# Optimization experiments

Hardware: AMD Instinct MI355X
Metric: run time of the kernel (lower is better)

The kernel has to match this reference:

```python
import jax, jax.numpy as jnp
import numpy as np

H, D, C, K, N, B = 16, 64, 1024, 256, 4096, 2

def setup_inputs() -> dict:
    key = jax.random.key(0)
    ks = jax.random.split(key, 10)
    s = lambda k, shp, fan: jax.random.normal(k, shp, jnp.float32) * (1.0 / np.sqrt(fan))
    return {
        "x": jax.random.normal(ks[0], (B, N, C), jnp.float32),
        "Wq": s(ks[1], (H, D, C), C),   # per-head Linear(channels->dim), no bias
        "Wk": s(ks[2], (H, D, C), C),
        "Wv": s(ks[3], (H, D, C), C),
        "We": s(ks[4], (H, K, N), N),   # E: Linear(input_size->dim_k)
        "bE": jnp.zeros((H, K), jnp.float32),
        "Wf": s(ks[5], (H, K, N), N),   # F: Linear(input_size->dim_k)
        "bF": jnp.zeros((H, K), jnp.float32),
        "Wo": s(ks[6], (C, H * D), H * D),
        "bo": jnp.zeros((C,), jnp.float32),
    }

def reference(x, Wq, Wk, Wv, We, bE, Wf, bF, Wo, bo):
    b, n, c = x.shape
    h, d = Wq.shape[0], Wq.shape[1]
    # per-head Q/K/V projections, vectorized over heads: [b,h,n,d]
    Q = jnp.einsum('bnc,hdc->bhnd', x, Wq)
    Kt = jnp.einsum('bnc,hdc->bhdn', x, Wk)   # K already transposed(1,2)
    Vt = jnp.einsum('bnc,hdc->bhdn', x, Wv)   # V transposed(1,2)
    # Linformer E/F low-rank projections along sequence axis -> [b,h,d,k]
    Ke = jnp.einsum('bhdn,hkn->bhdk', Kt, We) + bE[None, :, None, :]
    Vf = jnp.einsum('bhdn,hkn->bhdk', Vt, Wf) + bF[None, :, None, :]
    # scaled scores + softmax over low-rank dim k
    scores = jnp.einsum('bhnd,bhdk->bhnk', Q, Kt if False else Ke) / jnp.sqrt(jnp.asarray(d, x.dtype))
    P = jax.nn.softmax(scores, axis=-1)
    # P @ V_f^T  -> [b,h,n,d]
    out = jnp.einsum('bhnk,bhkd->bhnd', P, jnp.swapaxes(Vf, -1, -2))
    # concat heads -> [b,n,h*d]
    out = jnp.transpose(out, (0, 2, 1, 3)).reshape(b, n, h * d)
    out = jax.nn.gelu(out, approximate=False)
    return out @ Wo.T + bo
```

## Files before the change

kernel.cpp:

```cpp
#include <hip/hip_runtime.h>

typedef unsigned short u16;
typedef float f32x4 __attribute__((ext_vector_type(4)));
typedef short s16x8 __attribute__((ext_vector_type(8)));
typedef unsigned short u16x4 __attribute__((ext_vector_type(4)));

__device__ __forceinline__ u16 f2bf(float f) {
  union { float f; unsigned u; } v; v.f = f;
  unsigned r = v.u + 0x7FFFu + ((v.u >> 16) & 1u);
  return (u16)(r >> 16);
}

__device__ __forceinline__ void gload_lds16(const void* g, void* l) {
  __builtin_amdgcn_global_load_lds(
      (const __attribute__((address_space(1))) void*)g,
      (__attribute__((address_space(3))) void*)l, 16, 0, 0);
}

__global__ __launch_bounds__(256) void cast_f32_bf16(
    const float* __restrict__ src, u16* __restrict__ dst, int n4) {
  int i = blockIdx.x * 256 + threadIdx.x;
  if (i >= n4) return;
  f32x4 v = ((const f32x4*)src)[i];
  u16x4 o = { f2bf(v[0]), f2bf(v[1]), f2bf(v[2]), f2bf(v[3]) };
  ((u16x4*)dst)[i] = o;
}

template <int FINAL>
__global__ __launch_bounds__(256) void gemm_bt(
    const u16* __restrict__ A, const u16* __restrict__ B,
    void* __restrict__ Cout, const float* __restrict__ bias,
    int K, int lda, int ldb, int ldc) {
  __shared__ u16 As[128 * 32];
  __shared__ u16 Bs[128 * 32];
  const int tid = threadIdx.x;
  const int wid = tid >> 6, lane = tid & 63;
  const int lo = lane & 15, hi = lane >> 4;
  const int wr = wid >> 1, wc = wid & 1;
  const long brow = (long)blockIdx.y * 128;
  const long bcol = (long)blockIdx.x * 128;

  f32x4 acc[4][4] = {};

  const char* Ab = (const char*)(A + (size_t)brow * lda);
  const char* Bb = (const char*)(B + (size_t)bcol * ldb);
  const int ldab = lda * 2, ldbb = ldb * 2;

  for (int k0 = 0; k0 < K; k0 += 32) {
#pragma unroll
    for (int i = 0; i < 2; ++i) {
      int ob = wid * 2048 + i * 1024;
      int o = ob + lane * 16;
      int row = o >> 6, cb = o & 63;
      gload_lds16(Ab + (size_t)row * ldab + k0 * 2 + cb, (char*)As + ob);
      gload_lds16(Bb + (size_t)row * ldbb + k0 * 2 + cb, (char*)Bs + ob);
    }
    __syncthreads();
    s16x8 af[4], bfr[4];
#pragma unroll
    for (int m = 0; m < 4; ++m)
      af[m] = *(const s16x8*)&As[(wr * 64 + m * 16 + lo) * 32 + hi * 8];
#pragma unroll
    for (int n = 0; n < 4; ++n)
      bfr[n] = *(const s16x8*)&Bs[(wc * 64 + n * 16 + lo) * 32 + hi * 8];
#pragma unroll
    for (int m = 0; m < 4; ++m)
#pragma unroll
      for (int n = 0; n < 4; ++n)
        acc[m][n] = __builtin_amdgcn_mfma_f32_16x16x32_bf16(af[m], bfr[n], acc[m][n], 0, 0, 0);
    __syncthreads();
  }
#pragma unroll
  for (int m = 0; m < 4; ++m) {
#pragma unroll
    for (int n = 0; n < 4; ++n) {
#pragma unroll
      for (int r = 0; r < 4; ++r) {
        size_t row = brow + wr * 64 + m * 16 + hi * 4 + r;
        size_t col = bcol + wc * 64 + n * 16 + lo;
        float v = acc[m][n][r];
        if (FINAL) ((float*)Cout)[row * ldc + col] = v + bias[col];
        else       ((u16*)Cout)[row * ldc + col] = f2bf(v);
      }
    }
  }
}

__global__ __launch_bounds__(256) void kevf_kernel(
    const float* __restrict__ We, const float* __restrict__ Wf,
    const u16* __restrict__ QKV, float* __restrict__ part) {
  __shared__ u16 Wa[64 * 32];
  __shared__ u16 Vt[64 * 32];
  const int type = blockIdx.z >> 2, ns = blockIdx.z & 3;
  const int bh = blockIdx.y, b = bh >> 4, h = bh & 15;
  const int kk0 = blockIdx.x * 64;
  const float* W = (type ? Wf : We) + ((size_t)(h * 256 + kk0)) * 4096;
  const int col0 = (type ? 2048 : 1024) + h * 64;
  const int tid = threadIdx.x, wid = tid >> 6, lane = tid & 63;
  const int lo = lane & 15, hi = lane >> 4;

  f32x4 acc[4] = {};

  const int nbeg = ns << 10, nend = nbeg + 1024;
  for (int n0 = nbeg; n0 < nend; n0 += 32) {
    {
      int r = tid >> 2, c8 = (tid & 3) * 8;
      const f32x4* wp = (const f32x4*)(W + (size_t)r * 4096 + n0 + c8);
      f32x4 v0 = wp[0], v1 = wp[1];
      s16x8 wv;
      wv[0] = (short)f2bf(v0[0]); wv[1] = (short)f2bf(v0[1]);
      wv[2] = (short)f2bf(v0[2]); wv[3] = (short)f2bf(v0[3]);
      wv[4] = (short)f2bf(v1[0]); wv[5] = (short)f2bf(v1[1]);
      wv[6] = (short)f2bf(v1[2]); wv[7] = (short)f2bf(v1[3]);
      *(s16x8*)((char*)Wa + r * 64 + ((c8 * 2) ^ ((r & 3) << 4))) = wv;
    }
    {
      int n = tid >> 3, dd0 = (tid & 7) * 8;
      s16x8 v = *(const s16x8*)(QKV + (size_t)(b * 4096 + n0 + n) * 3072 + col0 + dd0);
#pragma unroll
      for (int q = 0; q < 8; ++q) {
        int dd = dd0 + q;
        Vt[dd * 32 + (n ^ (((dd >> 3) & 3) << 3))] = (u16)v[q];
      }
    }
    __syncthreads();
    int rr = wid * 16 + lo;
    s16x8 a = *(const s16x8*)((const char*)Wa + rr * 64 + ((hi * 16) ^ ((rr & 3) << 4)));
#pragma unroll
    for (int dt = 0; dt < 4; ++dt) {
      int dd = dt * 16 + lo;
      s16x8 bv = *(const s16x8*)&Vt[dd * 32 + ((hi * 8) ^ (((dd >> 3) & 3) << 3))];
      acc[dt] = __builtin_amdgcn_mfma_f32_16x16x32_bf16(a, bv, acc[dt], 0, 0, 0);
    }
    __syncthreads();
  }
  const size_t pbase = ((size_t)((type * 32 + bh) * 4 + blockIdx.x) * 4 + ns) * 4096;
#pragma unroll
  for (int dt = 0; dt < 4; ++dt)
#pragma unroll
    for (int r = 0; r < 4; ++r) {
      int kkl = wid * 16 + hi * 4 + r;
      int dd = dt * 16 + lo;
      part[pbase + kkl * 64 + dd] = acc[dt][r];
    }
}

__global__ __launch_bounds__(256) void kevf_reduce(
    const float* __restrict__ part, const float* __restrict__ bE,
    const float* __restrict__ bF, u16* __restrict__ KeT, u16* __restrict__ Vf) {
  const int tb = blockIdx.x;
  const int type = tb >> 7, bh = (tb >> 2) & 31, kc = tb & 3;
  const int t = threadIdx.x;
  const int kkl = t >> 2, dd0 = (t & 3) * 16;
  const float* p = part + (size_t)tb * 16384 + kkl * 64 + dd0;
  f32x4 s[4];
#pragma unroll
  for (int j = 0; j < 4; ++j) s[j] = ((const f32x4*)p)[j];
#pragma unroll
  for (int ns = 1; ns < 4; ++ns)
#pragma unroll
    for (int j = 0; j < 4; ++j) {
      f32x4 v = ((const f32x4*)(p + ns * 4096))[j];
      s[j][0] += v[0]; s[j][1] += v[1]; s[j][2] += v[2]; s[j][3] += v[3];
    }
  const int kk = kc * 64 + kkl;
  const float bias = (type ? bF : bE)[(bh & 15) * 256 + kk];
  if (type == 0) {
    u16* o = KeT + ((size_t)bh * 256 + kk) * 64 + dd0;
#pragma unroll
    for (int j = 0; j < 4; ++j) {
      u16x4 w = { f2bf(s[j][0] + bias), f2bf(s[j][1] + bias),
                  f2bf(s[j][2] + bias), f2bf(s[j][3] + bias) };
      *(u16x4*)(o + j * 4) = w;
    }
  } else {
#pragma unroll
    for (int j = 0; j < 4; ++j)
#pragma unroll
      for (int e = 0; e < 4; ++e) {
        int dd = dd0 + j * 4 + e;
        Vf[((size_t)bh * 64 + dd) * 256 + kk] = f2bf(s[j][e] + bias);
      }
  }
}

__global__ __launch_bounds__(256) void attn_fused(
    const u16* __restrict__ QKV, const u16* __restrict__ KeT,
    const u16* __restrict__ Vf, u16* __restrict__ attn) {
  __shared__ char smem[65536];
  char* sKe = smem;
  char* sVf = smem + 32768;
  const int tid = threadIdx.x, wid = tid >> 6, lane = tid & 63;
  const int lo = lane & 15, hi = lane >> 4;
  const int bh = blockIdx.y, b = bh >> 4, h = bh & 15;
  const int n0 = blockIdx.x * 64;

  const char* keg = (const char*)(KeT + (size_t)bh * 256 * 64);
  const char* vfg = (const char*)(Vf + (size_t)bh * 64 * 256);
#pragma unroll
  for (int i = 0; i < 8; ++i) {
    int ob = wid * 8192 + i * 1024;
    int o = ob + lane * 16;
    int kr = o >> 7, kc = o & 127;
    gload_lds16(keg + kr * 128 + (kc ^ ((kr & 7) << 4)), sKe + ob);
    int vr = o >> 9, vc = o & 511;
    gload_lds16(vfg + vr * 512 + (vc ^ ((vr & 7) << 4)), sVf + ob);
  }
  const u16* qp = QKV + (size_t)(b * 4096 + n0 + wid * 16 + lo) * 3072 + h * 64;
  s16x8 qf0 = *(const s16x8*)(qp + hi * 8);
  s16x8 qf1 = *(const s16x8*)(qp + 32 + hi * 8);
  __syncthreads();

  f32x4 sc[16];
#pragma unroll
  for (int nt = 0; nt < 16; ++nt) {
    int kk = nt * 16 + lo;
    int sw = (kk & 7) << 4;
    s16x8 b0 = *(const s16x8*)(sKe + kk * 128 + ((hi * 16) ^ sw));
    s16x8 b1 = *(const s16x8*)(sKe + kk * 128 + ((64 + hi * 16) ^ sw));
    f32x4 c = {0.f, 0.f, 0.f, 0.f};
    c = __builtin_amdgcn_mfma_f32_16x16x32_bf16(qf0, b0, c, 0, 0, 0);
    c = __builtin_amdgcn_mfma_f32_16x16x32_bf16(qf1, b1, c, 0, 0, 0);
    sc[nt] = c;
  }
  float mx[4], inv[4];
#pragma unroll
  for (int r = 0; r < 4; ++r) {
    float m = sc[0][r];
#pragma unroll
    for (int nt = 1; nt < 16; ++nt) m = fmaxf(m, sc[nt][r]);
    m = fmaxf(m, __shfl_xor(m, 1));
    m = fmaxf(m, __shfl_xor(m, 2));
    m = fmaxf(m, __shfl_xor(m, 4));
    m = fmaxf(m, __shfl_xor(m, 8));
    mx[r] = m;
  }
  const float SCL = 0.125f * 1.4426950408889634f;
  float sm[4] = {0.f, 0.f, 0.f, 0.f};
#pragma unroll
  for (int nt = 0; nt < 16; ++nt)
#pragma unroll
    for (int r = 0; r < 4; ++r) {
      float p = exp2f((sc[nt][r] - mx[r]) * SCL);
      sc[nt][r] = p;
      sm[r] += p;
    }
#pragma unroll
  for (int r = 0; r < 4; ++r) {
    float s = sm[r];
    s += __shfl_xor(s, 1);
    s += __shfl_xor(s, 2);
    s += __shfl_xor(s, 4);
    s += __shfl_xor(s, 8);
    inv[r] = 1.0f / s;
  }
  __syncthreads();
  char* pb = smem + wid * 8192;
#pragma unroll
  for (int nt = 0; nt < 16; ++nt)
#pragma unroll
    for (int r = 0; r < 4; ++r) {
      int row = hi * 4 + r;
      int kk = nt * 16 + lo;
      *(u16*)(pb + row * 512 + ((kk * 2) ^ ((row & 7) << 4))) = f2bf(sc[nt][r] * inv[r]);
    }
  __syncthreads();
  s16x8 pa[8];
#pragma unroll
  for (int ks = 0; ks < 8; ++ks)
    pa[ks] = *(const s16x8*)(pb + lo * 512 + ((ks * 64 + hi * 16) ^ ((lo & 7) << 4)));
#pragma unroll
  for (int dt = 0; dt < 4; ++dt) {
    int dd = dt * 16 + lo;
    int sw = (dd & 7) << 4;
    f32x4 o = {0.f, 0.f, 0.f, 0.f};
#pragma unroll
    for (int ks = 0; ks < 8; ++ks) {
      s16x8 vb = *(const s16x8*)(sVf + dd * 512 + ((ks * 64 + hi * 16) ^ sw));
      o = __builtin_amdgcn_mfma_f32_16x16x32_bf16(pa[ks], vb, o, 0, 0, 0);
    }
#pragma unroll
    for (int r = 0; r < 4; ++r) {
      int row = n0 + wid * 16 + hi * 4 + r;
      float x = o[r];
      float g = 0.5f * x * (1.0f + erff(x * 0.7071067811865476f));
      attn[(size_t)(b * 4096 + row) * 1024 + h * 64 + dd] = f2bf(g);
    }
  }
}

extern "C" void kernel_launch(void* const* d_in, const int* in_sizes, int n_in,
                              void* d_out, int out_size, void* d_ws, size_t ws_size,
                              hipStream_t stream) {
  const float* x  = (const float*)d_in[0];
  const float* Wq = (const float*)d_in[1];
  const float* Wk = (const float*)d_in[2];
  const float* Wv = (const float*)d_in[3];
  const float* We = (const float*)d_in[4];
  const float* bE = (const float*)d_in[5];
  const float* Wf = (const float*)d_in[6];
  const float* bF = (const float*)d_in[7];
  const float* Wo = (const float*)d_in[8];
  const float* bo = (const float*)d_in[9];
  float* out = (float*)d_out;

  char* ws = (char*)d_ws;
  u16* xb   = (u16*)(ws);
  u16* Wqkv = (u16*)(ws + 16777216);
  u16* Wob  = (u16*)(ws + 23068672);
  u16* QKV  = (u16*)(ws + 25165824);
  u16* KeT  = (u16*)(ws + 75497472);
  u16* Vf   = (u16*)(ws + 76546048);
  u16* attn = (u16*)(ws + 77594624);
  float* part = (float*)(ws);

  cast_f32_bf16<<<8192, 256, 0, stream>>>(x, xb, 2097152);
  cast_f32_bf16<<<1024, 256, 0, stream>>>(Wq, Wqkv, 262144);
  cast_f32_bf16<<<1024, 256, 0, stream>>>(Wk, Wqkv + 1048576, 262144);
  cast_f32_bf16<<<1024, 256, 0, stream>>>(Wv, Wqkv + 2097152, 262144);
  cast_f32_bf16<<<1024, 256, 0, stream>>>(Wo, Wob, 262144);

  gemm_bt<0><<<dim3(24, 64), 256, 0, stream>>>(xb, Wqkv, QKV, nullptr,
                                               1024, 1024, 1024, 3072);
  kevf_kernel<<<dim3(4, 32, 8), 256, 0, stream>>>(We, Wf, QKV, part);
  kevf_reduce<<<256, 256, 0, stream>>>(part, bE, bF, KeT, Vf);
  attn_fused<<<dim3(64, 32), 256, 0, stream>>>(QKV, KeT, Vf, attn);
  gemm_bt<1><<<dim3(8, 64), 256, 0, stream>>>(attn, Wob, out, bo,
                                              1024, 1024, 1024, 1024);
}
```

Measured before the change: 223.7 us.

## Replace GEMM with 4-stage pipelined, swizzled LDS kernel using 128x256 tiles

Replaces the synchronous single-buffer bf16 GEMM with a 4-stage ring of LDS buffers. Three k-tiles are prefetched ahead via global_load_lds, with vmcnt waits and a single barrier per iteration. The block tile grows to 128x256 with 8 waves, and an XOR swizzle on LDS column offsets is meant to reduce bank conflicts on fragment reads. The goal is to hide global-load latency behind MFMA work in the QKV and output projections, at the cost of more LDS per block and fewer blocks in flight.

```diff
diff --git a/kernel.cpp b/kernel.cpp
--- a/kernel.cpp
+++ b/kernel.cpp
@@ -27,57 +27,92 @@
 }
 
 template <int FINAL>
-__global__ __launch_bounds__(256) void gemm_bt(
+__global__ __launch_bounds__(512) void gemm_pipe(
     const u16* __restrict__ A, const u16* __restrict__ B,
     void* __restrict__ Cout, const float* __restrict__ bias,
     int K, int lda, int ldb, int ldc) {
-  __shared__ u16 As[128 * 32];
-  __shared__ u16 Bs[128 * 32];
+  __shared__ char smem[4 * 8192 + 4 * 16384];
+  char* sA = smem;
+  char* sB = smem + 32768;
   const int tid = threadIdx.x;
   const int wid = tid >> 6, lane = tid & 63;
   const int lo = lane & 15, hi = lane >> 4;
-  const int wr = wid >> 1, wc = wid & 1;
+  const int wm = wid >> 2, wn = wid & 3;
   const long brow = (long)blockIdx.y * 128;
-  const long bcol = (long)blockIdx.x * 128;
+  const long bcol = (long)blockIdx.x * 256;
+  const int T = K >> 5;
 
   f32x4 acc[4][4] = {};
 
   const char* Ab = (const char*)(A + (size_t)brow * lda);
   const char* Bb = (const char*)(B + (size_t)bcol * ldb);
-  const int ldab = lda * 2, ldbb = ldb * 2;
-
-  for (int k0 = 0; k0 < K; k0 += 32) {
-#pragma unroll
-    for (int i = 0; i < 2; ++i) {
-      int ob = wid * 2048 + i * 1024;
-      int o = ob + lane * 16;
-      int row = o >> 6, cb = o & 63;
-      gload_lds16(Ab + (size_t)row * ldab + k0 * 2 + cb, (char*)As + ob);
-      gload_lds16(Bb + (size_t)row * ldbb + k0 * 2 + cb, (char*)Bs + ob);
-    }
-    __syncthreads();
-    s16x8 af[4], bfr[4];
+  const size_t ldab = (size_t)lda * 2, ldbb = (size_t)ldb * 2;
+
+  const int aoff = wid * 1024 + lane * 16;
+  const int arow = aoff >> 6, acb = aoff & 63;
+  const char* asrc = Ab + (size_t)arow * ldab + (acb ^ ((arow & 3) << 4));
+  const int boff0 = (wid * 2) * 1024 + lane * 16;
+  const int brw0 = boff0 >> 6, bcb0 = boff0 & 63;
+  const char* bsrc0 = Bb + (size_t)brw0 * ldbb + (bcb0 ^ ((brw0 & 3) << 4));
+  const int boff1 = (wid * 2 + 1) * 1024 + lane * 16;
+  const int brw1 = boff1 >> 6, bcb1 = boff1 & 63;
+  const char* bsrc1 = Bb + (size_t)brw1 * ldbb + (bcb1 ^ ((brw1 & 3) << 4));
+
+  int ra[4], rb[4];
+#pragma unroll
+  for (int m = 0; m < 4; ++m)
+    ra[m] = (wm * 64 + m * 16 + lo) * 64 + ((hi * 16) ^ ((lo & 3) << 4));
+#pragma unroll
+  for (int n = 0; n < 4; ++n)
+    rb[n] = (wn * 64 + n * 16 + lo) * 64 + ((hi * 16) ^ ((lo & 3) << 4));
+
+#define STAGE(t)                                                         \
+  {                                                                      \
+    int s_ = (t) & 3;                                                    \
+    size_t kb_ = (size_t)(t) << 6;                                       \
+    gload_lds16(asrc + kb_, sA + s_ * 8192 + wid * 1024);                \
+    gload_lds16(bsrc0 + kb_, sB + s_ * 16384 + wid * 2048);              \
+    gload_lds16(bsrc1 + kb_, sB + s_ * 16384 + wid * 2048 + 1024);       \
+  }
+
+  STAGE(0); STAGE(1); STAGE(2);
+  asm volatile("s_waitcnt vmcnt(6)" ::: "memory");
+  __builtin_amdgcn_s_barrier();
+  __builtin_amdgcn_sched_barrier(0);
+
+  for (int t = 0; t < T; ++t) {
+    const char* bufA = sA + (t & 3) * 8192;
+    const char* bufB = sB + (t & 3) * 16384;
+    s16x8 af[4], bf[4];
+#pragma unroll
+    for (int m = 0; m < 4; ++m) af[m] = *(const s16x8*)(bufA + ra[m]);
+#pragma unroll
+    for (int n = 0; n < 4; ++n) bf[n] = *(const s16x8*)(bufB + rb[n]);
+    if (t + 3 < T) STAGE(t + 3);
+    __builtin_amdgcn_s_setprio(1);
 #pragma unroll
     for (int m = 0; m < 4; ++m)
-      af[m] = *(const s16x8*)&As[(wr * 64 + m * 16 + lo) * 32 + hi * 8];
-#pragma unroll
-    for (int n = 0; n < 4; ++n)
-      bfr[n] = *(const s16x8*)&Bs[(wc * 64 + n * 16 + lo) * 32 + hi * 8];
-#pragma unroll
-    for (int m = 0; m < 4; ++m)
 #pragma unroll
       for (int n = 0; n < 4; ++n)
-        acc[m][n] = __builtin_amdgcn_mfma_f32_16x16x32_bf16(af[m], bfr[n], acc[m][n], 0, 0, 0);
-    __syncthreads();
-  }
+        acc[m][n] = __builtin_amdgcn_mfma_f32_16x16x32_bf16(af[m], bf[n], acc[m][n], 0, 0, 0);
+    __builtin_amdgcn_s_setprio(0);
+    int rem = T - 2 - t;
+    if (rem >= 2)      asm volatile("s_waitcnt vmcnt(6)" ::: "memory");
+    else if (rem == 1) asm volatile("s_waitcnt vmcnt(3)" ::: "memory");
+    else               asm volatile("s_waitcnt vmcnt(0)" ::: "memory");
+    __builtin_amdgcn_s_barrier();
+    __builtin_amdgcn_sched_barrier(0);
+  }
+#undef STAGE
+
 #pragma unroll
   for (int m = 0; m < 4; ++m) {
 #pragma unroll
     for (int n = 0; n < 4; ++n) {
 #pragma unroll
       for (int r = 0; r < 4; ++r) {
-        size_t row = brow + wr * 64 + m * 16 + hi * 4 + r;
-        size_t col = bcol + wc * 64 + n * 16 + lo;
+        size_t row = brow + wm * 64 + m * 16 + hi * 4 + r;
+        size_t col = bcol + wn * 64 + n * 16 + lo;
         float v = acc[m][n][r];
         if (FINAL) ((float*)Cout)[row * ldc + col] = v + bias[col];
         else       ((u16*)Cout)[row * ldc + col] = f2bf(v);
@@ -320,11 +355,11 @@
   cast_f32_bf16<<<1024, 256, 0, stream>>>(Wv, Wqkv + 2097152, 262144);
   cast_f32_bf16<<<1024, 256, 0, stream>>>(Wo, Wob, 262144);
 
-  gemm_bt<0><<<dim3(24, 64), 256, 0, stream>>>(xb, Wqkv, QKV, nullptr,
-                                               1024, 1024, 1024, 3072);
+  gemm_pipe<0><<<dim3(12, 64), 512, 0, stream>>>(xb, Wqkv, QKV, nullptr,
+                                                 1024, 1024, 1024, 3072);
   kevf_kernel<<<dim3(4, 32, 8), 256, 0, stream>>>(We, Wf, QKV, part);
   kevf_reduce<<<256, 256, 0, stream>>>(part, bE, bF, KeT, Vf);
   attn_fused<<<dim3(64, 32), 256, 0, stream>>>(QKV, KeT, Vf, attn);
-  gemm_bt<1><<<dim3(8, 64), 256, 0, stream>>>(attn, Wob, out, bo,
-                                              1024, 1024, 1024, 1024);
-}
+  gemm_pipe<1><<<dim3(4, 64), 512, 0, stream>>>(attn, Wob, out, bo,
+                                                1024, 1024, 1024, 1024);
+}
```

New measurement: 220.9 us. No clear change (-1.3%).

## Pipeline GEMM with triple-buffered LDS and 128x256 tiles; prefetch kevf loads

Applied to the files above, without the earlier changes.

Replaces the bf16 GEMM with a 128x256-tile kernel that keeps three swizzled LDS stages in flight via async global-to-LDS loads. It uses explicit vmcnt waits and a single barrier per k-step, which removes the two full syncs per iteration and the bank conflicts. The kevf kernel now prefetches three iterations of W and QKV into registers, processes 64 sequence elements per step and double-buffers the transposed V tile in LDS. The trade is higher register and LDS use, which lowers occupancy, and fewer blocks for the output GEMM (256).

```diff
diff --git a/kernel.cpp b/kernel.cpp
--- a/kernel.cpp
+++ b/kernel.cpp
@@ -27,57 +27,98 @@
 }
 
 template <int FINAL>
-__global__ __launch_bounds__(256) void gemm_bt(
+__global__ __launch_bounds__(256, 2) void gemm_pipe(
     const u16* __restrict__ A, const u16* __restrict__ B,
     void* __restrict__ Cout, const float* __restrict__ bias,
     int K, int lda, int ldb, int ldc) {
-  __shared__ u16 As[128 * 32];
-  __shared__ u16 Bs[128 * 32];
+  __shared__ char smem[3 * 8192 + 3 * 16384];
   const int tid = threadIdx.x;
   const int wid = tid >> 6, lane = tid & 63;
   const int lo = lane & 15, hi = lane >> 4;
   const int wr = wid >> 1, wc = wid & 1;
   const long brow = (long)blockIdx.y * 128;
-  const long bcol = (long)blockIdx.x * 128;
-
-  f32x4 acc[4][4] = {};
+  const long bcol = (long)blockIdx.x * 256;
+  const int T = K >> 5;
+
+  f32x4 acc[4][8] = {};
 
   const char* Ab = (const char*)(A + (size_t)brow * lda);
   const char* Bb = (const char*)(B + (size_t)bcol * ldb);
-  const int ldab = lda * 2, ldbb = ldb * 2;
-
-  for (int k0 = 0; k0 < K; k0 += 32) {
-#pragma unroll
-    for (int i = 0; i < 2; ++i) {
-      int ob = wid * 2048 + i * 1024;
-      int o = ob + lane * 16;
-      int row = o >> 6, cb = o & 63;
-      gload_lds16(Ab + (size_t)row * ldab + k0 * 2 + cb, (char*)As + ob);
-      gload_lds16(Bb + (size_t)row * ldbb + k0 * 2 + cb, (char*)Bs + ob);
-    }
-    __syncthreads();
-    s16x8 af[4], bfr[4];
+  const size_t ldab = (size_t)lda * 2, ldbb = (size_t)ldb * 2;
+
+  const int LA0 = wid * 2048 + lane * 16, LA1 = LA0 + 1024;
+  const int LB0 = wid * 4096 + lane * 16, LB1 = LB0 + 1024;
+  const int LB2 = LB0 + 2048, LB3 = LB0 + 3072;
+#define SRCCOL(L) (((L) & 63) ^ ((((L) >> 7) & 3) << 4))
+  const char* aS0 = Ab + (size_t)(LA0 >> 6) * ldab + SRCCOL(LA0);
+  const char* aS1 = Ab + (size_t)(LA1 >> 6) * ldab + SRCCOL(LA1);
+  const char* bS0 = Bb + (size_t)(LB0 >> 6) * ldbb + SRCCOL(LB0);
+  const char* bS1 = Bb + (size_t)(LB1 >> 6) * ldbb + SRCCOL(LB1);
+  const char* bS2 = Bb + (size_t)(LB2 >> 6) * ldbb + SRCCOL(LB2);
+  const char* bS3 = Bb + (size_t)(LB3 >> 6) * ldbb + SRCCOL(LB3);
+#undef SRCCOL
+
+  int ra[4], rb[8];
+#pragma unroll
+  for (int m = 0; m < 4; ++m) {
+    int row = wr * 64 + m * 16 + lo;
+    ra[m] = row * 64 + ((hi ^ ((row >> 1) & 3)) << 4);
+  }
+#pragma unroll
+  for (int n = 0; n < 8; ++n) {
+    int row = wc * 128 + n * 16 + lo;
+    rb[n] = row * 64 + ((hi ^ ((row >> 1) & 3)) << 4);
+  }
+
+#define STAGE(t)                                                    \
+  {                                                                 \
+    char* sa_ = smem + ((t) % 3) * 8192;                            \
+    char* sb_ = smem + 24576 + ((t) % 3) * 16384;                   \
+    size_t kb_ = (size_t)(t) << 6;                                  \
+    gload_lds16(aS0 + kb_, sa_ + LA0);                              \
+    gload_lds16(aS1 + kb_, sa_ + LA1);                              \
+    gload_lds16(bS0 + kb_, sb_ + LB0);                              \
+    gload_lds16(bS1 + kb_, sb_ + LB1);                              \
+    gload_lds16(bS2 + kb_, sb_ + LB2);                              \
+    gload_lds16(bS3 + kb_, sb_ + LB3);                              \
+  }
+
+  STAGE(0); STAGE(1);
+  asm volatile("s_waitcnt vmcnt(6)" ::: "memory");
+  __builtin_amdgcn_s_barrier();
+  __builtin_amdgcn_sched_barrier(0);
+
+  for (int t = 0; t < T; ++t) {
+    const char* sa = smem + (t % 3) * 8192;
+    const char* sb = smem + 24576 + (t % 3) * 16384;
+    s16x8 af[4], bf[8];
+#pragma unroll
+    for (int m = 0; m < 4; ++m) af[m] = *(const s16x8*)(sa + ra[m]);
+#pragma unroll
+    for (int n = 0; n < 8; ++n) bf[n] = *(const s16x8*)(sb + rb[n]);
+    if (t + 2 < T) STAGE(t + 2);
+    __builtin_amdgcn_s_setprio(1);
 #pragma unroll
     for (int m = 0; m < 4; ++m)
-      af[m] = *(const s16x8*)&As[(wr * 64 + m * 16 + lo) * 32 + hi * 8];
-#pragma unroll
-    for (int n = 0; n < 4; ++n)
-      bfr[n] = *(const s16x8*)&Bs[(wc * 64 + n * 16 + lo) * 32 + hi * 8];
-#pragma unroll
-    for (int m = 0; m < 4; ++m)
-#pragma unroll
-      for (int n = 0; n < 4; ++n)
-        acc[m][n] = __builtin_amdgcn_mfma_f32_16x16x32_bf16(af[m], bfr[n], acc[m][n], 0, 0, 0);
-    __syncthreads();
-  }
+#pragma unroll
+      for (int n = 0; n < 8; ++n)
+        acc[m][n] = __builtin_amdgcn_mfma_f32_16x16x32_bf16(af[m], bf[n], acc[m][n], 0, 0, 0);
+    __builtin_amdgcn_s_setprio(0);
+    if (t + 2 < T) asm volatile("s_waitcnt vmcnt(6)" ::: "memory");
+    else           asm volatile("s_waitcnt vmcnt(0)" ::: "memory");
+    __builtin_amdgcn_s_barrier();
+    __builtin_amdgcn_sched_barrier(0);
+  }
+#undef STAGE
+
 #pragma unroll
   for (int m = 0; m < 4; ++m) {
 #pragma unroll
-    for (int n = 0; n < 4; ++n) {
+    for (int n = 0; n < 8; ++n) {
 #pragma unroll
       for (int r = 0; r < 4; ++r) {
         size_t row = brow + wr * 64 + m * 16 + hi * 4 + r;
-        size_t col = bcol + wc * 64 + n * 16 + lo;
+        size_t col = bcol + wc * 128 + n * 16 + lo;
         float v = acc[m][n][r];
         if (FINAL) ((float*)Cout)[row * ldc + col] = v + bias[col];
         else       ((u16*)Cout)[row * ldc + col] = f2bf(v);
@@ -89,8 +130,7 @@
 __global__ __launch_bounds__(256) void kevf_kernel(
     const float* __restrict__ We, const float* __restrict__ Wf,
     const u16* __restrict__ QKV, float* __restrict__ part) {
-  __shared__ u16 Wa[64 * 32];
-  __shared__ u16 Vt[64 * 32];
+  __shared__ u16 Vt[2][64 * 64];
   const int type = blockIdx.z >> 2, ns = blockIdx.z & 3;
   const int bh = blockIdx.y, b = bh >> 4, h = bh & 15;
   const int kk0 = blockIdx.x * 64;
@@ -98,50 +138,68 @@
   const int col0 = (type ? 2048 : 1024) + h * 64;
   const int tid = threadIdx.x, wid = tid >> 6, lane = tid & 63;
   const int lo = lane & 15, hi = lane >> 4;
+  const int nbeg = ns << 10;
+
+  const int rr = wid * 16 + lo;
+  const float* wsrc = W + (size_t)rr * 4096 + nbeg + hi * 8;
+  const int qn = tid >> 2, qc = (tid & 3) * 16;
+  const u16* qsrc = QKV + ((size_t)b * 4096 + nbeg + qn) * 3072 + col0 + qc;
 
   f32x4 acc[4] = {};
-
-  const int nbeg = ns << 10, nend = nbeg + 1024;
-  for (int n0 = nbeg; n0 < nend; n0 += 32) {
-    {
-      int r = tid >> 2, c8 = (tid & 3) * 8;
-      const f32x4* wp = (const f32x4*)(W + (size_t)r * 4096 + n0 + c8);
-      f32x4 v0 = wp[0], v1 = wp[1];
-      s16x8 wv;
-      wv[0] = (short)f2bf(v0[0]); wv[1] = (short)f2bf(v0[1]);
-      wv[2] = (short)f2bf(v0[2]); wv[3] = (short)f2bf(v0[3]);
-      wv[4] = (short)f2bf(v1[0]); wv[5] = (short)f2bf(v1[1]);
-      wv[6] = (short)f2bf(v1[2]); wv[7] = (short)f2bf(v1[3]);
-      *(s16x8*)((char*)Wa + r * 64 + ((c8 * 2) ^ ((r & 3) << 4))) = wv;
-    }
-    {
-      int n = tid >> 3, dd0 = (tid & 7) * 8;
-      s16x8 v = *(const s16x8*)(QKV + (size_t)(b * 4096 + n0 + n) * 3072 + col0 + dd0);
-#pragma unroll
-      for (int q = 0; q < 8; ++q) {
-        int dd = dd0 + q;
-        Vt[dd * 32 + (n ^ (((dd >> 3) & 3) << 3))] = (u16)v[q];
-      }
-    }
+  f32x4 w[3][4];
+  s16x8 q[3][2];
+
+#define KISSUE(t) {                                       \
+    const float* wp_ = wsrc + (size_t)(t) * 64;           \
+    w[(t) % 3][0] = *(const f32x4*)wp_;                   \
+    w[(t) % 3][1] = *(const f32x4*)(wp_ + 4);             \
+    w[(t) % 3][2] = *(const f32x4*)(wp_ + 32);            \
+    w[(t) % 3][3] = *(const f32x4*)(wp_ + 36);            \
+    const u16* qp_ = qsrc + (size_t)(t) * 64 * 3072;      \
+    q[(t) % 3][0] = *(const s16x8*)qp_;                   \
+    q[(t) % 3][1] = *(const s16x8*)(qp_ + 8); }
+
+  KISSUE(0); KISSUE(1); KISSUE(2);
+#pragma unroll
+  for (int t = 0; t < 16; ++t) {
+    u16* vb = Vt[t & 1];
+#pragma unroll
+    for (int e = 0; e < 16; ++e) {
+      int dd = qc + e;
+      int sw = (dd & 7) ^ ((dd >> 4) & 3);
+      u16 val = (e < 8) ? (u16)q[t % 3][0][e] : (u16)q[t % 3][1][e - 8];
+      vb[dd * 64 + (qn ^ (sw << 3))] = val;
+    }
+    s16x8 a0, a1;
+#pragma unroll
+    for (int j = 0; j < 4; ++j) {
+      a0[j]     = (short)f2bf(w[t % 3][0][j]);
+      a0[j + 4] = (short)f2bf(w[t % 3][1][j]);
+      a1[j]     = (short)f2bf(w[t % 3][2][j]);
+      a1[j + 4] = (short)f2bf(w[t % 3][3][j]);
+    }
+    if (t + 3 < 16) KISSUE(t + 3);
     __syncthreads();
-    int rr = wid * 16 + lo;
-    s16x8 a = *(const s16x8*)((const char*)Wa + rr * 64 + ((hi * 16) ^ ((rr & 3) << 4)));
 #pragma unroll
     for (int dt = 0; dt < 4; ++dt) {
       int dd = dt * 16 + lo;
-      s16x8 bv = *(const s16x8*)&Vt[dd * 32 + ((hi * 8) ^ (((dd >> 3) & 3) << 3))];
-      acc[dt] = __builtin_amdgcn_mfma_f32_16x16x32_bf16(a, bv, acc[dt], 0, 0, 0);
-    }
-    __syncthreads();
-  }
+      int sw = (lo & 7) ^ dt;
+      s16x8 b0 = *(const s16x8*)&vb[dd * 64 + ((hi * 8) ^ (sw << 3))];
+      s16x8 b1 = *(const s16x8*)&vb[dd * 64 + ((32 + hi * 8) ^ (sw << 3))];
+      acc[dt] = __builtin_amdgcn_mfma_f32_16x16x32_bf16(a0, b0, acc[dt], 0, 0, 0);
+      acc[dt] = __builtin_amdgcn_mfma_f32_16x16x32_bf16(a1, b1, acc[dt], 0, 0, 0);
+    }
+  }
+#undef KISSUE
+
   const size_t pbase = ((size_t)((type * 32 + bh) * 4 + blockIdx.x) * 4 + ns) * 4096;
 #pragma unroll
   for (int dt = 0; dt < 4; ++dt)
 #pragma unroll
-    for (int r = 0; r < 4; ++r) {
-      int kkl = wid * 16 + hi * 4 + r;
+    for (int rg = 0; rg < 4; ++rg) {
+      int kkl = wid * 16 + hi * 4 + rg;
       int dd = dt * 16 + lo;
-      part[pbase + kkl * 64 + dd] = acc[dt][r];
+      part[pbase + kkl * 64 + dd] = acc[dt][rg];
     }
 }
 
@@ -320,11 +378,11 @@
   cast_f32_bf16<<<1024, 256, 0, stream>>>(Wv, Wqkv + 2097152, 262144);
   cast_f32_bf16<<<1024, 256, 0, stream>>>(Wo, Wob, 262144);
 
-  gemm_bt<0><<<dim3(24, 64), 256, 0, stream>>>(xb, Wqkv, QKV, nullptr,
-                                               1024, 1024, 1024, 3072);
+  gemm_pipe<0><<<dim3(12, 64), 256, 0, stream>>>(xb, Wqkv, QKV, nullptr,
+                                                 1024, 1024, 1024, 3072);
   kevf_kernel<<<dim3(4, 32, 8), 256, 0, stream>>>(We, Wf, QKV, part);
   kevf_reduce<<<256, 256, 0, stream>>>(part, bE, bF, KeT, Vf);
   attn_fused<<<dim3(64, 32), 256, 0, stream>>>(QKV, KeT, Vf, attn);
-  gemm_bt<1><<<dim3(8, 64), 256, 0, stream>>>(attn, Wob, out, bo,
-                                              1024, 1024, 1024, 1024);
-}
+  gemm_pipe<1><<<dim3(4, 64), 256, 0, stream>>>(attn, Wob, out, bo,
+                                                1024, 1024, 1024, 1024);
+}
```

Measured after the change: 200.6 us. 1.12x faster.
